# Kernel tuning notes

Hardware: AMD Instinct MI355X
Metric: run time of the kernel (lower is better)

The kernel has to match this reference:

```python
import jax, jax.numpy as jnp
import numpy as np

NUM_DENSE = 13
NUM_SPARSE = 26
FEAT_NUM = 40000  # categories per sparse field
FEATURE_LENGTH = NUM_SPARSE * FEAT_NUM + NUM_DENSE  # 1_040_013
K = 64
BATCH = 4096


def setup_inputs() -> dict:
    key = jax.random.key(0)
    k1, k2, k3, k4 = jax.random.split(key, 4)
    dense_inputs = jax.random.normal(k1, (BATCH, NUM_DENSE), dtype=jnp.float32)
    sparse_inputs = jax.random.randint(k2, (BATCH, NUM_SPARSE), 0, FEAT_NUM, dtype=jnp.int64)
    w0 = jnp.zeros((1,), dtype=jnp.float32)
    w = jax.random.normal(k3, (FEATURE_LENGTH, 1), dtype=jnp.float32) * 0.05
    V = jax.random.normal(k4, (K, FEATURE_LENGTH), dtype=jnp.float32) * 0.05
    return {"dense_inputs": dense_inputs, "sparse_inputs": sparse_inputs, "w0": w0, "w": w, "V": V}


def reference(dense_inputs, sparse_inputs, w0, w, V):
    # Feature layout matches the original concat order: [dense (NUM_DENSE) | one-hot field 0 | ... | one-hot field 25].
    # The one-hot @ matrix products are computed as row gathers (mathematically identical,
    # since one_hot(i) @ M == M[i]).
    offsets = NUM_DENSE + FEAT_NUM * jnp.arange(NUM_SPARSE, dtype=sparse_inputs.dtype)
    idx = sparse_inputs + offsets[None, :]  # [B, NUM_SPARSE] global row ids into feature_length

    # ---- first order: w0 + stack @ w ----
    w_dense = w[:NUM_DENSE]            # [ND, 1]
    first = w0 + dense_inputs @ w_dense + jnp.sum(w[idx, 0], axis=1, keepdims=True)  # [B,1]

    # ---- second order: 0.5 * sum((stack @ V^T)^2 - (stack^2 @ (V^T)^2), axis=1) ----
    Vt = V.T                           # [F, K]
    Vt_dense = Vt[:NUM_DENSE]          # [ND, K]
    Vt_sparse = Vt[idx]                # [B, NUM_SPARSE, K] gathered latent vectors

    sv = dense_inputs @ Vt_dense + jnp.sum(Vt_sparse, axis=1)                 # [B, K]
    # stack^2 for the one-hot block equals the one-hot block itself (0/1 entries)
    s2v2 = (dense_inputs ** 2) @ (Vt_dense ** 2) + jnp.sum(Vt_sparse ** 2, axis=1)  # [B, K]

    second = 0.5 * jnp.sum(sv ** 2 - s2v2, axis=1, keepdims=True)  # [B,1]
    return first + second
```

## Files before the change

kernel.cpp:

```cpp
#include <hip/hip_runtime.h>

#define NUM_DENSE 13
#define NUM_SPARSE 26
#define FEAT_NUM 40000
#define FEATURE_LENGTH (NUM_SPARSE * FEAT_NUM + NUM_DENSE)
#define KDIM 64
#define BATCH 4096
#define QSIZE 8000
#define NCHUNK 5
#define LDSN (QSIZE + 4)
#define NT 1024

__global__ void transpose_kernel(const int* __restrict__ sp, int* __restrict__ sp_t) {
    int tid = blockIdx.x * blockDim.x + threadIdx.x;
    int j = tid >> 12;
    int b = tid & 4095;
    sp_t[tid] = sp[b * NUM_SPARSE + j];
}

__global__ __launch_bounds__(NT) void accum_kernel(const float* __restrict__ V,
                                                   const int* __restrict__ sp_t,
                                                   float* __restrict__ PS,
                                                   float* __restrict__ PQ) {
    __shared__ __align__(16) float buf[2][LDSN];

    const int k = blockIdx.x;
    const int g = blockIdx.y;
    const int jstart = (g * NUM_SPARSE) / 4;
    const int jend   = ((g + 1) * NUM_SPARSE) / 4;
    const int tid = threadIdx.x;

    const size_t kbase = (size_t)k * FEATURE_LENGTH + NUM_DENSE;
    const int a   = (int)(kbase & 3);
    const int nl4 = (QSIZE + a + 3) >> 2;

    const int nstage = (jend - jstart) * NCHUNK;

    float sAcc[4] = {0.f, 0.f, 0.f, 0.f};
    float qAcc[4] = {0.f, 0.f, 0.f, 0.f};

    int j = jstart, q = 0;
    int spv[4];
#pragma unroll
    for (int r = 0; r < 4; ++r) spv[r] = sp_t[j * BATCH + tid + NT * r];

    {
        const float4* __restrict__ g4 =
            (const float4*)(V + (kbase + (size_t)j * FEAT_NUM) - a);
        float4 v0 = g4[tid];
        bool p1 = (tid + NT) < nl4;
        float4 v1;
        if (p1) v1 = g4[tid + NT];
        *reinterpret_cast<float4*>(&buf[0][4 * tid]) = v0;
        if (p1) *reinterpret_cast<float4*>(&buf[0][4 * (tid + NT)]) = v1;
    }
    __syncthreads();

    int cur = 0;
    for (int s = 0; s < nstage; ++s) {
        int qn = q + 1, jn = j;
        if (qn == NCHUNK) { qn = 0; jn = j + 1; }
        const bool hasNext = (s + 1 < nstage);

        float4 v0, v1;
        bool p1 = false;
        if (hasNext) {
            const float4* __restrict__ g4 =
                (const float4*)(V + (kbase + (size_t)jn * FEAT_NUM + (size_t)qn * QSIZE) - a);
            v0 = g4[tid];
            p1 = (tid + NT) < nl4;
            if (p1) v1 = g4[tid + NT];
        }

        {
            const int q0 = q * QSIZE;
#pragma unroll
            for (int r = 0; r < 4; ++r) {
                int rel = spv[r] - q0;
                bool in = (rel >= 0) && (rel < QSIZE);
                int addr = in ? (rel + a) : 0;
                float v = buf[cur][addr];
                v = in ? v : 0.f;
                sAcc[r] += v;
                qAcc[r] += v * v;
            }
        }

        if (hasNext) {
            *reinterpret_cast<float4*>(&buf[cur ^ 1][4 * tid]) = v0;
            if (p1) *reinterpret_cast<float4*>(&buf[cur ^ 1][4 * (tid + NT)]) = v1;
        }
        __syncthreads();
        cur ^= 1;

        if (hasNext && jn != j) {
#pragma unroll
            for (int r = 0; r < 4; ++r) spv[r] = sp_t[jn * BATCH + tid + NT * r];
        }
        j = jn; q = qn;
    }

    const int base = (g * KDIM + k) * BATCH + tid;
#pragma unroll
    for (int r = 0; r < 4; ++r) {
        PS[base + NT * r] = sAcc[r];
        PQ[base + NT * r] = qAcc[r];
    }
}

__global__ __launch_bounds__(256) void final_kernel(const float* __restrict__ dense,
                                                    const float* __restrict__ w0,
                                                    const float* __restrict__ w,
                                                    const float* __restrict__ V,
                                                    const int* __restrict__ sp_t,
                                                    const float* __restrict__ PS,
                                                    const float* __restrict__ PQ,
                                                    float* __restrict__ out) {
    __shared__ float red[4][64];
    const int wv = threadIdx.x >> 6;
    const int ln = threadIdx.x & 63;
    const int b  = blockIdx.x * 64 + ln;

    float x[NUM_DENSE], x2[NUM_DENSE];
#pragma unroll
    for (int d = 0; d < NUM_DENSE; ++d) {
        x[d]  = dense[b * NUM_DENSE + d];
        x2[d] = x[d] * x[d];
    }

    float t = 0.f;
    const int k0 = wv * 16;
#pragma unroll 4
    for (int kk = 0; kk < 16; ++kk) {
        const int k = k0 + kk;
        float sv = 0.f, qv = 0.f;
#pragma unroll
        for (int g = 0; g < 4; ++g) {
            sv += PS[((g << 6) + k) * BATCH + b];
            qv += PQ[((g << 6) + k) * BATCH + b];
        }
        const float* __restrict__ Vk = V + (size_t)k * FEATURE_LENGTH;
#pragma unroll
        for (int d = 0; d < NUM_DENSE; ++d) {
            float vv = Vk[d];
            sv += x[d] * vv;
            qv += x2[d] * vv * vv;
        }
        t += sv * sv - qv;
    }
    t *= 0.5f;

    for (int jj = wv; jj < NUM_SPARSE; jj += 4)
        t += w[NUM_DENSE + jj * FEAT_NUM + sp_t[jj * BATCH + b]];
    if (wv == 0) {
#pragma unroll
        for (int d = 0; d < NUM_DENSE; ++d) t += x[d] * w[d];
    }

    red[wv][ln] = t;
    __syncthreads();
    if (wv == 0)
        out[b] = w0[0] + red[0][ln] + red[1][ln] + red[2][ln] + red[3][ln];
}

extern "C" void kernel_launch(void* const* d_in, const int* in_sizes, int n_in,
                              void* d_out, int out_size, void* d_ws, size_t ws_size,
                              hipStream_t stream) {
    const float* dense  = (const float*)d_in[0];
    const int*   sparse = (const int*)d_in[1];
    const float* w0     = (const float*)d_in[2];
    const float* w      = (const float*)d_in[3];
    const float* V      = (const float*)d_in[4];
    float* out = (float*)d_out;

    char* ws = (char*)d_ws;
    int*   sp_t = (int*)ws;
    float* PS   = (float*)(ws + (1 << 19));
    float* PQ   = (float*)(ws + (1 << 19) + 4 * KDIM * BATCH * 4);

    transpose_kernel<<<(NUM_SPARSE * BATCH) / 256, 256, 0, stream>>>(sparse, sp_t);
    accum_kernel<<<dim3(KDIM, 4), NT, 0, stream>>>(V, sp_t, PS, PQ);
    final_kernel<<<BATCH / 64, 256, 0, stream>>>(dense, w0, w, V, sp_t, PS, PQ, out);
}
```

Before: 401.2 us.

## Use direct global-to-LDS loads, split sparse fields over 8 groups, restructure final reduction

The streaming loads of V chunks now go straight into shared memory through the AMD global_load_lds builtin instead of passing through registers. The sparse fields are split across 8 block groups instead of 4, so 512 blocks run instead of 256 and each SM sees more work. The final kernel is reorganised so each block handles 16 batch rows, with each thread covering 4 latent dimensions before a shared-memory reduction. This costs a larger partial-sum buffer and more partial reads in the final kernel. The direct LDS loads also rely on the builtin's per-lane addressing matching the float4 layout.

```diff
diff --git a/kernel.cpp b/kernel.cpp
--- a/kernel.cpp
+++ b/kernel.cpp
@@ -10,12 +10,19 @@
 #define NCHUNK 5
 #define LDSN (QSIZE + 4)
 #define NT 1024
+#define NG 8
 
 __global__ void transpose_kernel(const int* __restrict__ sp, int* __restrict__ sp_t) {
     int tid = blockIdx.x * blockDim.x + threadIdx.x;
     int j = tid >> 12;
     int b = tid & 4095;
     sp_t[tid] = sp[b * NUM_SPARSE + j];
+}
+
+__device__ __forceinline__ void load_lds16(const float4* g, float* l) {
+    __builtin_amdgcn_global_load_lds(
+        (const __attribute__((address_space(1))) void*)g,
+        (__attribute__((address_space(3))) void*)l, 16, 0, 0);
 }
 
 __global__ __launch_bounds__(NT) void accum_kernel(const float* __restrict__ V,
@@ -26,14 +33,13 @@
 
     const int k = blockIdx.x;
     const int g = blockIdx.y;
-    const int jstart = (g * NUM_SPARSE) / 4;
-    const int jend   = ((g + 1) * NUM_SPARSE) / 4;
     const int tid = threadIdx.x;
+    const int jstart = (g * NUM_SPARSE) / NG;
+    const int jend   = ((g + 1) * NUM_SPARSE) / NG;
 
     const size_t kbase = (size_t)k * FEATURE_LENGTH + NUM_DENSE;
     const int a   = (int)(kbase & 3);
     const int nl4 = (QSIZE + a + 3) >> 2;
-
     const int nstage = (jend - jstart) * NCHUNK;
 
     float sAcc[4] = {0.f, 0.f, 0.f, 0.f};
@@ -47,12 +53,8 @@
     {
         const float4* __restrict__ g4 =
             (const float4*)(V + (kbase + (size_t)j * FEAT_NUM) - a);
-        float4 v0 = g4[tid];
-        bool p1 = (tid + NT) < nl4;
-        float4 v1;
-        if (p1) v1 = g4[tid + NT];
-        *reinterpret_cast<float4*>(&buf[0][4 * tid]) = v0;
-        if (p1) *reinterpret_cast<float4*>(&buf[0][4 * (tid + NT)]) = v1;
+        load_lds16(g4 + tid, &buf[0][4 * tid]);
+        if (1024 + tid < nl4) load_lds16(g4 + 1024 + tid, &buf[0][4 * (1024 + tid)]);
     }
     __syncthreads();
 
@@ -62,14 +64,12 @@
         if (qn == NCHUNK) { qn = 0; jn = j + 1; }
         const bool hasNext = (s + 1 < nstage);
 
-        float4 v0, v1;
-        bool p1 = false;
         if (hasNext) {
             const float4* __restrict__ g4 =
                 (const float4*)(V + (kbase + (size_t)jn * FEAT_NUM + (size_t)qn * QSIZE) - a);
-            v0 = g4[tid];
-            p1 = (tid + NT) < nl4;
-            if (p1) v1 = g4[tid + NT];
+            float* lb = &buf[cur ^ 1][0];
+            load_lds16(g4 + tid, lb + 4 * tid);
+            if (1024 + tid < nl4) load_lds16(g4 + 1024 + tid, lb + 4 * (1024 + tid));
         }
 
         {
@@ -86,18 +86,13 @@
             }
         }
 
-        if (hasNext) {
-            *reinterpret_cast<float4*>(&buf[cur ^ 1][4 * tid]) = v0;
-            if (p1) *reinterpret_cast<float4*>(&buf[cur ^ 1][4 * (tid + NT)]) = v1;
-        }
         __syncthreads();
-        cur ^= 1;
 
         if (hasNext && jn != j) {
 #pragma unroll
             for (int r = 0; r < 4; ++r) spv[r] = sp_t[jn * BATCH + tid + NT * r];
         }
-        j = jn; q = qn;
+        j = jn; q = qn; cur ^= 1;
     }
 
     const int base = (g * KDIM + k) * BATCH + tid;
@@ -116,10 +111,11 @@
                                                     const float* __restrict__ PS,
                                                     const float* __restrict__ PQ,
                                                     float* __restrict__ out) {
-    __shared__ float red[4][64];
-    const int wv = threadIdx.x >> 6;
-    const int ln = threadIdx.x & 63;
-    const int b  = blockIdx.x * 64 + ln;
+    __shared__ float red[16][17];
+    const int tid = threadIdx.x;
+    const int bi  = tid & 15;
+    const int ki  = tid >> 4;
+    const int b   = blockIdx.x * 16 + bi;
 
     float x[NUM_DENSE], x2[NUM_DENSE];
 #pragma unroll
@@ -129,13 +125,12 @@
     }
 
     float t = 0.f;
-    const int k0 = wv * 16;
-#pragma unroll 4
-    for (int kk = 0; kk < 16; ++kk) {
-        const int k = k0 + kk;
+#pragma unroll
+    for (int kk = 0; kk < 4; ++kk) {
+        const int k = ki * 4 + kk;
         float sv = 0.f, qv = 0.f;
 #pragma unroll
-        for (int g = 0; g < 4; ++g) {
+        for (int g = 0; g < NG; ++g) {
             sv += PS[((g << 6) + k) * BATCH + b];
             qv += PQ[((g << 6) + k) * BATCH + b];
         }
@@ -148,19 +143,21 @@
         }
         t += sv * sv - qv;
     }
-    t *= 0.5f;
+    red[bi][ki] = 0.5f * t;
+    __syncthreads();
 
-    for (int jj = wv; jj < NUM_SPARSE; jj += 4)
-        t += w[NUM_DENSE + jj * FEAT_NUM + sp_t[jj * BATCH + b]];
-    if (wv == 0) {
+    if (tid < 16) {
+        const int bb = blockIdx.x * 16 + tid;
+        float acc = w0[0];
 #pragma unroll
-        for (int d = 0; d < NUM_DENSE; ++d) t += x[d] * w[d];
+        for (int i = 0; i < 16; ++i) acc += red[tid][i];
+#pragma unroll
+        for (int j = 0; j < NUM_SPARSE; ++j)
+            acc += w[NUM_DENSE + j * FEAT_NUM + sp_t[j * BATCH + bb]];
+#pragma unroll
+        for (int d = 0; d < NUM_DENSE; ++d) acc += x[d] * w[d];
+        out[bb] = acc;
     }
-
-    red[wv][ln] = t;
-    __syncthreads();
-    if (wv == 0)
-        out[b] = w0[0] + red[0][ln] + red[1][ln] + red[2][ln] + red[3][ln];
 }
 
 extern "C" void kernel_launch(void* const* d_in, const int* in_sizes, int n_in,
@@ -175,10 +172,10 @@
 
     char* ws = (char*)d_ws;
     int*   sp_t = (int*)ws;
-    float* PS   = (float*)(ws + (1 << 19));
-    float* PQ   = (float*)(ws + (1 << 19) + 4 * KDIM * BATCH * 4);
+    float* PS   = (float*)(ws + (1 << 20));
+    float* PQ   = (float*)(ws + (1 << 20) + NG * KDIM * BATCH * 4);
 
     transpose_kernel<<<(NUM_SPARSE * BATCH) / 256, 256, 0, stream>>>(sparse, sp_t);
-    accum_kernel<<<dim3(KDIM, 4), NT, 0, stream>>>(V, sp_t, PS, PQ);
-    final_kernel<<<BATCH / 64, 256, 0, stream>>>(dense, w0, w, V, sp_t, PS, PQ, out);
+    accum_kernel<<<dim3(KDIM, NG), NT, 0, stream>>>(V, sp_t, PS, PQ);
+    final_kernel<<<BATCH / 16, 256, 0, stream>>>(dense, w0, w, V, sp_t, PS, PQ, out);
 }
```

After: 391.8 us. -2.3%, faster.
